# Kernel optimization log

Measured on AMD Instinct MI355X. Metric: run time of the kernel, lower is better.

## Reference

```python
import jax, jax.numpy as jnp
import numpy as np

H = 512          # hidden_size
B = 1024         # batch
T = 256          # warmup sequence length
NUM_STEPS = 64


def setup_inputs() -> dict:
    key = jax.random.key(0)
    ks = jax.random.split(key, 8)
    bound = 1.0 / np.sqrt(H)  # torch default init for RNN/Linear
    x = jax.random.normal(ks[0], (B, T), dtype=jnp.float32)
    W_ih = jax.random.uniform(ks[1], (H, 1), jnp.float32, -bound, bound)
    W_hh = jax.random.uniform(ks[2], (H, H), jnp.float32, -bound, bound)
    b_ih = jax.random.uniform(ks[3], (H,), jnp.float32, -bound, bound)
    b_hh = jax.random.uniform(ks[4], (H,), jnp.float32, -bound, bound)
    W_fc = jax.random.uniform(ks[5], (1, H), jnp.float32, -bound, bound)
    b_fc = jax.random.uniform(ks[6], (1,), jnp.float32, -bound, bound)
    return {"x": x, "W_ih": W_ih, "W_hh": W_hh, "b_ih": b_ih,
            "b_hh": b_hh, "W_fc": W_fc, "b_fc": b_fc, "num_steps": NUM_STEPS}


def reference(x, W_ih, W_hh, b_ih, b_hh, W_fc, b_fc, num_steps):
    # Phase 1: warmup RNN over the input series. h_t = relu(x_t*W_ih + b_ih + h@W_hh^T + b_hh)
    bias = b_ih + b_hh  # [H]
    w_in = W_ih[:, 0]   # [H], input_size == 1

    def warm_step(h, xt):                      # h: [B,H], xt: [B]
        h = jax.nn.relu(xt[:, None] * w_in[None, :] + h @ W_hh.T + bias)
        return h, None

    h0 = jnp.zeros((B, H), dtype=x.dtype)
    h, _ = jax.lax.scan(warm_step, h0, x.T)    # scan over time: x.T is [T,B]

    def roll_step(h, _):
        y = h @ W_fc.T + b_fc                  # [B,1]
        h = jax.nn.relu(y @ W_ih.T + h @ W_hh.T + bias)
        return h, y

    _, ys = jax.lax.scan(roll_step, h, None, length=num_steps)  # ys: [S,B,1]
    return jnp.transpose(ys, (1, 0, 2))        # [B, num_steps, 1]
```

## Files before the change

kernel.cpp:

```cpp
#include <hip/hip_runtime.h>
#include <stdint.h>

#define H 512
#define B_SZ 1024
#define T_WARM 256
#define NSTEPS 64
#define TOTAL_T (T_WARM + NSTEPS)

#define RPB 16
#define HC 128
#define NTEAM 64
#define NCG 4
#define NBLK 256
#define NTHR 512

typedef __attribute__((ext_vector_type(8))) short bf16x8;
typedef __attribute__((ext_vector_type(4))) float f32x4;

union u64x2_bf {
    uint64_t u[2];
    bf16x8 v;
};

__device__ __forceinline__ ushort f2bf(float f) {
    uint32_t u = __builtin_bit_cast(uint32_t, f);
    u += 0x7FFFu + ((u >> 16) & 1u);
    return (ushort)(u >> 16);
}
__device__ __forceinline__ float bf2f(ushort h) {
    uint32_t u = ((uint32_t)h) << 16;
    return __builtin_bit_cast(float, u);
}

__global__ void prep_kernel(const float* __restrict__ x,
                            const float* __restrict__ W_hh,
                            const float* __restrict__ b_ih,
                            const float* __restrict__ b_hh,
                            ushort* __restrict__ Wh, ushort* __restrict__ Wl,
                            float* __restrict__ bias, float* __restrict__ xT,
                            uint32_t* __restrict__ Hhi0, uint32_t* __restrict__ Hlo0,
                            uint32_t* __restrict__ flags) {
    int i = blockIdx.x * 512 + threadIdx.x;
    if (i < B_SZ * 256) { Hhi0[i] = 0u; Hlo0[i] = 0u; }
    if (i < 4096) flags[i] = 0u;
    if (i < H * H) {
        float w = W_hh[i];
        ushort hi = f2bf(w);
        float rem = w - bf2f(hi);
        Wh[i] = hi;
        Wl[i] = f2bf(rem);
    }
    if (i < B_SZ * T_WARM) {
        int b = i & (B_SZ - 1), t = i >> 10;
        xT[t * B_SZ + b] = x[b * T_WARM + t];
    }
    if (i < H) bias[i] = b_ih[i] + b_hh[i];
}

__global__ __launch_bounds__(NTHR, 1)
void rnn_kernel(const float* __restrict__ xT,
                const float* __restrict__ W_ih,
                const float* __restrict__ b_fc_p,
                const float* __restrict__ W_fc,
                const ushort* __restrict__ Wh_g,
                const ushort* __restrict__ Wl_g,
                const float* __restrict__ bias_g,
                uint32_t* __restrict__ Hhi0, uint32_t* __restrict__ Hhi1,
                uint32_t* __restrict__ Hlo0, uint32_t* __restrict__ Hlo1,
                uint32_t* __restrict__ flags,
                float* __restrict__ out) {
    __shared__ float pc[8 * 8 * 64 * 4];
    __shared__ float w_fc_s[H];
    __shared__ float w_in_s[HC];
    __shared__ float bias_s[HC];
    __shared__ float ypt[32 * 16];
    __shared__ float sx[RPB];
    __shared__ float sy[RPB];

    const int tid = threadIdx.x;
    const int bid = blockIdx.x;
    const int team = bid & (NTEAM - 1);
    const int cg = bid >> 6;
    const int row0 = team * RPB;
    const int col0 = cg * HC;

    w_fc_s[tid] = W_fc[tid];
    if (tid < HC) { w_in_s[tid] = W_ih[col0 + tid]; bias_s[tid] = bias_g[col0 + tid]; }
    const float bfc = b_fc_p[0];

    const int lane = tid & 63;
    const int wv = tid >> 6;
    const int n = lane & 15, q = lane >> 4;

    bf16x8 Bh[16], Bl[16];
    {
        const int kb = wv * 64 + q * 8;
        #pragma unroll
        for (int c = 0; c < 8; ++c) {
            const ushort* wh = Wh_g + (col0 + c * 16 + n) * H + kb;
            const ushort* wl = Wl_g + (col0 + c * 16 + n) * H + kb;
            Bh[c * 2 + 0] = *(const bf16x8*)(wh);
            Bh[c * 2 + 1] = *(const bf16x8*)(wh + 32);
            Bl[c * 2 + 0] = *(const bf16x8*)(wl);
            Bl[c * 2 + 1] = *(const bf16x8*)(wl + 32);
        }
    }

    uint32_t* myflag = flags + (team * NCG + cg) * 16;
    const uint32_t* pollflag = flags + (team * NCG + (wv >> 1)) * 16;
    const bool selfw = ((wv >> 1) == cg);

    for (int t = 0; t < TOTAL_T; ++t) {
        float xv = 0.f;
        if (t < T_WARM && tid < RPB) xv = xT[t * B_SZ + row0 + tid];

        if (t > 0 && !selfw) {
            while (__hip_atomic_load(pollflag, __ATOMIC_RELAXED, __HIP_MEMORY_SCOPE_AGENT)
                   < (uint32_t)t)
                __builtin_amdgcn_s_sleep(1);
        }

        const uint64_t* ph = (const uint64_t*)((t & 1) ? Hhi1 : Hhi0);
        const uint64_t* pl = (const uint64_t*)((t & 1) ? Hlo1 : Hlo0);
        const int abase = (row0 + n) * 128 + wv * 16 + q * 2;
        u64x2_bf ah[2], al[2];
        #pragma unroll
        for (int ktl = 0; ktl < 2; ++ktl) {
            ah[ktl].u[0] = __hip_atomic_load(ph + abase + ktl * 8 + 0, __ATOMIC_RELAXED, __HIP_MEMORY_SCOPE_AGENT);
            ah[ktl].u[1] = __hip_atomic_load(ph + abase + ktl * 8 + 1, __ATOMIC_RELAXED, __HIP_MEMORY_SCOPE_AGENT);
            al[ktl].u[0] = __hip_atomic_load(pl + abase + ktl * 8 + 0, __ATOMIC_RELAXED, __HIP_MEMORY_SCOPE_AGENT);
            al[ktl].u[1] = __hip_atomic_load(pl + abase + ktl * 8 + 1, __ATOMIC_RELAXED, __HIP_MEMORY_SCOPE_AGENT);
        }

        f32x4 acc[8];
        #pragma unroll
        for (int c = 0; c < 8; ++c) acc[c] = (f32x4){0.f, 0.f, 0.f, 0.f};
        #pragma unroll
        for (int ktl = 0; ktl < 2; ++ktl) {
            #pragma unroll
            for (int c = 0; c < 8; ++c) {
                acc[c] = __builtin_amdgcn_mfma_f32_16x16x32_bf16(ah[ktl].v, Bh[c * 2 + ktl], acc[c], 0, 0, 0);
                acc[c] = __builtin_amdgcn_mfma_f32_16x16x32_bf16(al[ktl].v, Bh[c * 2 + ktl], acc[c], 0, 0, 0);
                acc[c] = __builtin_amdgcn_mfma_f32_16x16x32_bf16(ah[ktl].v, Bl[c * 2 + ktl], acc[c], 0, 0, 0);
            }
        }

        #pragma unroll
        for (int c = 0; c < 8; ++c)
            *(f32x4*)(&pc[((wv * 8 + c) * 64 + lane) * 4]) = acc[c];
        if (t < T_WARM && tid < RPB) sx[tid] = xv;
        if (t >= T_WARM) {
            float yp = 0.f;
            #pragma unroll
            for (int ktl = 0; ktl < 2; ++ktl)
                #pragma unroll
                for (int j = 0; j < 8; ++j) {
                    int k = wv * 64 + ktl * 32 + q * 8 + j;
                    yp += (bf2f((ushort)ah[ktl].v[j]) + bf2f((ushort)al[ktl].v[j])) * w_fc_s[k];
                }
            ypt[(wv * 4 + q) * 16 + n] = yp;
        }
        __syncthreads();

        if (t >= T_WARM) {
            if (tid < RPB) {
                float s = bfc;
                #pragma unroll
                for (int g = 0; g < 32; ++g) s += ypt[g * 16 + tid];
                sy[tid] = s;
                if (cg == 0) out[(row0 + tid) * NSTEPS + (t - T_WARM)] = s;
            }
            __syncthreads();
        }

        f32x4 v = (f32x4){0.f, 0.f, 0.f, 0.f};
        #pragma unroll
        for (int w = 0; w < 8; ++w)
            v += *(const f32x4*)(&pc[((w * 8 + wv) * 64 + lane) * 4]);

        const int jl = wv * 16 + n;
        const float wi = w_in_s[jl], bj = bias_s[jl];
        uint32_t* dsth = ((t & 1) ? Hhi0 : Hhi1);
        uint32_t* dstl = ((t & 1) ? Hlo0 : Hlo1);
        const int pi = (col0 + jl) >> 1;
        #pragma unroll
        for (int i = 0; i < 4; ++i) {
            int m = q * 4 + i;
            float sv = (t < T_WARM) ? sx[m] : sy[m];
            float val = v[i] + sv * wi + bj;
            val = fmaxf(val, 0.f);
            ushort hi = f2bf(val);
            float rem = val - bf2f(hi);
            uint32_t mine = ((uint32_t)hi << 16) | (uint32_t)f2bf(rem);
            uint32_t partner = (uint32_t)__shfl_xor((int)mine, 1);
            int du = (row0 + m) * 256 + pi;
            if ((n & 1) == 0) {
                uint32_t hw = (mine >> 16) | (partner & 0xFFFF0000u);
                __hip_atomic_store(dsth + du, hw, __ATOMIC_RELAXED, __HIP_MEMORY_SCOPE_AGENT);
            } else {
                uint32_t lw = (partner & 0xFFFFu) | (mine << 16);
                __hip_atomic_store(dstl + du, lw, __ATOMIC_RELAXED, __HIP_MEMORY_SCOPE_AGENT);
            }
        }
        __syncthreads();
        if (tid == 0)
            __hip_atomic_store(myflag, (uint32_t)(t + 1), __ATOMIC_RELAXED, __HIP_MEMORY_SCOPE_AGENT);
    }
}

extern "C" void kernel_launch(void* const* d_in, const int* in_sizes, int n_in,
                              void* d_out, int out_size, void* d_ws, size_t ws_size,
                              hipStream_t stream) {
    const float* x    = (const float*)d_in[0];
    const float* W_ih = (const float*)d_in[1];
    const float* W_hh = (const float*)d_in[2];
    const float* b_ih = (const float*)d_in[3];
    const float* b_hh = (const float*)d_in[4];
    const float* W_fc = (const float*)d_in[5];
    const float* b_fc = (const float*)d_in[6];
    float* out = (float*)d_out;

    uint8_t* w = (uint8_t*)d_ws;
    ushort*   Wh    = (ushort*)(w);
    ushort*   Wl    = (ushort*)(w + 524288);
    float*    bias  = (float*)(w + 1048576);
    float*    xT    = (float*)(w + 1052672);
    uint32_t* Hhi0  = (uint32_t*)(w + 2101248);
    uint32_t* Hhi1  = (uint32_t*)(w + 3149824);
    uint32_t* Hlo0  = (uint32_t*)(w + 4198400);
    uint32_t* Hlo1  = (uint32_t*)(w + 5246976);
    uint32_t* flags = (uint32_t*)(w + 6295552);

    prep_kernel<<<1024, 512, 0, stream>>>(x, W_hh, b_ih, b_hh, Wh, Wl, bias, xT, Hhi0, Hlo0, flags);
    rnn_kernel<<<NBLK, NTHR, 0, stream>>>(xT, W_ih, b_fc, W_fc, Wh, Wl, bias,
                                          Hhi0, Hhi1, Hlo0, Hlo1, flags, out);
}
```

Measured before the change: 1.173 ms.

## Replace per-step flag barrier with tag-bit-validated hidden state polling

Drops the separate per-block progress flags and the trailing block barrier. Each hidden-state word now carries a parity tag in its top bit, and consumers spin on the data itself until every word shows the expected tag. The partial-sum LDS buffer is double-buffered to remove the end-of-step syncthreads, and x is broadcast by shuffle instead of through shared memory. This cuts a flag round-trip and a barrier from every step. In exchange the tag bit overwrites the sign bit of the hi/lo words, which relies on relu outputs being non-negative and on the residual's sign being recoverable, and state is stored unpacked and then repacked in registers.

```diff
diff --git a/kernel.cpp b/kernel.cpp
--- a/kernel.cpp
+++ b/kernel.cpp
@@ -17,10 +17,7 @@
 typedef __attribute__((ext_vector_type(8))) short bf16x8;
 typedef __attribute__((ext_vector_type(4))) float f32x4;
 
-union u64x2_bf {
-    uint64_t u[2];
-    bf16x8 v;
-};
+union u32x4_bf { uint32_t w[4]; bf16x8 v; };
 
 __device__ __forceinline__ ushort f2bf(float f) {
     uint32_t u = __builtin_bit_cast(uint32_t, f);
@@ -38,11 +35,10 @@
                             const float* __restrict__ b_hh,
                             ushort* __restrict__ Wh, ushort* __restrict__ Wl,
                             float* __restrict__ bias, float* __restrict__ xT,
-                            uint32_t* __restrict__ Hhi0, uint32_t* __restrict__ Hlo0,
-                            uint32_t* __restrict__ flags) {
+                            uint32_t* __restrict__ Hb0, uint32_t* __restrict__ Hb1) {
     int i = blockIdx.x * 512 + threadIdx.x;
-    if (i < B_SZ * 256) { Hhi0[i] = 0u; Hlo0[i] = 0u; }
-    if (i < 4096) flags[i] = 0u;
+    Hb0[i] = 0u;
+    Hb1[i] = 0x80000000u;
     if (i < H * H) {
         float w = W_hh[i];
         ushort hi = f2bf(w);
@@ -65,16 +61,13 @@
                 const ushort* __restrict__ Wh_g,
                 const ushort* __restrict__ Wl_g,
                 const float* __restrict__ bias_g,
-                uint32_t* __restrict__ Hhi0, uint32_t* __restrict__ Hhi1,
-                uint32_t* __restrict__ Hlo0, uint32_t* __restrict__ Hlo1,
-                uint32_t* __restrict__ flags,
+                uint32_t* __restrict__ Hb0, uint32_t* __restrict__ Hb1,
                 float* __restrict__ out) {
-    __shared__ float pc[8 * 8 * 64 * 4];
+    __shared__ float pc[2][8 * 8 * 64 * 4];
     __shared__ float w_fc_s[H];
     __shared__ float w_in_s[HC];
     __shared__ float bias_s[HC];
     __shared__ float ypt[32 * 16];
-    __shared__ float sx[RPB];
     __shared__ float sy[RPB];
 
     const int tid = threadIdx.x;
@@ -106,49 +99,59 @@
         }
     }
 
-    uint32_t* myflag = flags + (team * NCG + cg) * 16;
-    const uint32_t* pollflag = flags + (team * NCG + (wv >> 1)) * 16;
-    const bool selfw = ((wv >> 1) == cg);
+    const uint64_t TB = 0x8000000080000000ULL;
 
     for (int t = 0; t < TOTAL_T; ++t) {
         float xv = 0.f;
-        if (t < T_WARM && tid < RPB) xv = xT[t * B_SZ + row0 + tid];
-
-        if (t > 0 && !selfw) {
-            while (__hip_atomic_load(pollflag, __ATOMIC_RELAXED, __HIP_MEMORY_SCOPE_AGENT)
-                   < (uint32_t)t)
-                __builtin_amdgcn_s_sleep(1);
-        }
-
-        const uint64_t* ph = (const uint64_t*)((t & 1) ? Hhi1 : Hhi0);
-        const uint64_t* pl = (const uint64_t*)((t & 1) ? Hlo1 : Hlo0);
-        const int abase = (row0 + n) * 128 + wv * 16 + q * 2;
-        u64x2_bf ah[2], al[2];
-        #pragma unroll
-        for (int ktl = 0; ktl < 2; ++ktl) {
-            ah[ktl].u[0] = __hip_atomic_load(ph + abase + ktl * 8 + 0, __ATOMIC_RELAXED, __HIP_MEMORY_SCOPE_AGENT);
-            ah[ktl].u[1] = __hip_atomic_load(ph + abase + ktl * 8 + 1, __ATOMIC_RELAXED, __HIP_MEMORY_SCOPE_AGENT);
-            al[ktl].u[0] = __hip_atomic_load(pl + abase + ktl * 8 + 0, __ATOMIC_RELAXED, __HIP_MEMORY_SCOPE_AGENT);
-            al[ktl].u[1] = __hip_atomic_load(pl + abase + ktl * 8 + 1, __ATOMIC_RELAXED, __HIP_MEMORY_SCOPE_AGENT);
-        }
+        if (t < T_WARM && lane < RPB) xv = xT[t * B_SZ + row0 + lane];
+
+        const uint64_t* src = (const uint64_t*)((t & 1) ? Hb1 : Hb0);
+        const int base = (row0 + n) * 256 + wv * 32 + q * 4;
+        const uint64_t want = ((t >> 1) & 1) ? TB : 0ULL;
+        uint64_t d[8];
+        for (;;) {
+            #pragma unroll
+            for (int j = 0; j < 4; ++j)
+                d[j] = __hip_atomic_load(src + base + j, __ATOMIC_RELAXED, __HIP_MEMORY_SCOPE_AGENT);
+            #pragma unroll
+            for (int j = 0; j < 4; ++j)
+                d[4 + j] = __hip_atomic_load(src + base + 16 + j, __ATOMIC_RELAXED, __HIP_MEMORY_SCOPE_AGENT);
+            uint64_t bad = 0;
+            #pragma unroll
+            for (int j = 0; j < 8; ++j) bad |= (d[j] ^ want);
+            if (__all((bad & TB) == 0)) break;
+            __builtin_amdgcn_s_sleep(1);
+        }
+        #pragma unroll
+        for (int j = 0; j < 8; ++j) d[j] &= ~TB;
+
+        u32x4_bf ah[2], al[2];
+        #pragma unroll
+        for (int ktl = 0; ktl < 2; ++ktl)
+            #pragma unroll
+            for (int p = 0; p < 4; ++p) {
+                uint32_t lo32 = (uint32_t)d[ktl * 4 + p];
+                uint32_t hi32 = (uint32_t)(d[ktl * 4 + p] >> 32);
+                ah[ktl].w[p] = (lo32 >> 16) | (hi32 & 0xFFFF0000u);
+                al[ktl].w[p] = (lo32 & 0xFFFFu) | (hi32 << 16);
+            }
 
         f32x4 acc[8];
         #pragma unroll
         for (int c = 0; c < 8; ++c) acc[c] = (f32x4){0.f, 0.f, 0.f, 0.f};
         #pragma unroll
-        for (int ktl = 0; ktl < 2; ++ktl) {
+        for (int ktl = 0; ktl < 2; ++ktl)
             #pragma unroll
             for (int c = 0; c < 8; ++c) {
                 acc[c] = __builtin_amdgcn_mfma_f32_16x16x32_bf16(ah[ktl].v, Bh[c * 2 + ktl], acc[c], 0, 0, 0);
                 acc[c] = __builtin_amdgcn_mfma_f32_16x16x32_bf16(al[ktl].v, Bh[c * 2 + ktl], acc[c], 0, 0, 0);
                 acc[c] = __builtin_amdgcn_mfma_f32_16x16x32_bf16(ah[ktl].v, Bl[c * 2 + ktl], acc[c], 0, 0, 0);
             }
-        }
-
+
+        float* pcb = pc[t & 1];
         #pragma unroll
         for (int c = 0; c < 8; ++c)
-            *(f32x4*)(&pc[((wv * 8 + c) * 64 + lane) * 4]) = acc[c];
-        if (t < T_WARM && tid < RPB) sx[tid] = xv;
+            *(f32x4*)(&pcb[((wv * 8 + c) * 64 + lane) * 4]) = acc[c];
         if (t >= T_WARM) {
             float yp = 0.f;
             #pragma unroll
@@ -176,35 +179,24 @@
         f32x4 v = (f32x4){0.f, 0.f, 0.f, 0.f};
         #pragma unroll
         for (int w = 0; w < 8; ++w)
-            v += *(const f32x4*)(&pc[((w * 8 + wv) * 64 + lane) * 4]);
+            v += *(const f32x4*)(&pcb[((w * 8 + wv) * 64 + lane) * 4]);
 
         const int jl = wv * 16 + n;
         const float wi = w_in_s[jl], bj = bias_s[jl];
-        uint32_t* dsth = ((t & 1) ? Hhi0 : Hhi1);
-        uint32_t* dstl = ((t & 1) ? Hlo0 : Hlo1);
-        const int pi = (col0 + jl) >> 1;
+        uint32_t* dst = ((t & 1) ? Hb0 : Hb1);
+        const uint32_t tagw = (((t + 1) >> 1) & 1) ? 0x80000000u : 0u;
         #pragma unroll
         for (int i = 0; i < 4; ++i) {
             int m = q * 4 + i;
-            float sv = (t < T_WARM) ? sx[m] : sy[m];
+            float sv = (t < T_WARM) ? __shfl(xv, m) : sy[m];
             float val = v[i] + sv * wi + bj;
             val = fmaxf(val, 0.f);
             ushort hi = f2bf(val);
             float rem = val - bf2f(hi);
-            uint32_t mine = ((uint32_t)hi << 16) | (uint32_t)f2bf(rem);
-            uint32_t partner = (uint32_t)__shfl_xor((int)mine, 1);
-            int du = (row0 + m) * 256 + pi;
-            if ((n & 1) == 0) {
-                uint32_t hw = (mine >> 16) | (partner & 0xFFFF0000u);
-                __hip_atomic_store(dsth + du, hw, __ATOMIC_RELAXED, __HIP_MEMORY_SCOPE_AGENT);
-            } else {
-                uint32_t lw = (partner & 0xFFFFu) | (mine << 16);
-                __hip_atomic_store(dstl + du, lw, __ATOMIC_RELAXED, __HIP_MEMORY_SCOPE_AGENT);
-            }
-        }
-        __syncthreads();
-        if (tid == 0)
-            __hip_atomic_store(myflag, (uint32_t)(t + 1), __ATOMIC_RELAXED, __HIP_MEMORY_SCOPE_AGENT);
+            uint32_t u = (((uint32_t)hi << 16) | (uint32_t)f2bf(rem)) | tagw;
+            __hip_atomic_store(dst + (row0 + m) * H + col0 + jl, u,
+                               __ATOMIC_RELAXED, __HIP_MEMORY_SCOPE_AGENT);
+        }
     }
 }
 
@@ -221,17 +213,13 @@
     float* out = (float*)d_out;
 
     uint8_t* w = (uint8_t*)d_ws;
-    ushort*   Wh    = (ushort*)(w);
-    ushort*   Wl    = (ushort*)(w + 524288);
-    float*    bias  = (float*)(w + 1048576);
-    float*    xT    = (float*)(w + 1052672);
-    uint32_t* Hhi0  = (uint32_t*)(w + 2101248);
-    uint32_t* Hhi1  = (uint32_t*)(w + 3149824);
-    uint32_t* Hlo0  = (uint32_t*)(w + 4198400);
-    uint32_t* Hlo1  = (uint32_t*)(w + 5246976);
-    uint32_t* flags = (uint32_t*)(w + 6295552);
-
-    prep_kernel<<<1024, 512, 0, stream>>>(x, W_hh, b_ih, b_hh, Wh, Wl, bias, xT, Hhi0, Hlo0, flags);
-    rnn_kernel<<<NBLK, NTHR, 0, stream>>>(xT, W_ih, b_fc, W_fc, Wh, Wl, bias,
-                                          Hhi0, Hhi1, Hlo0, Hlo1, flags, out);
-}
+    ushort*   Wh   = (ushort*)(w);
+    ushort*   Wl   = (ushort*)(w + 524288);
+    float*    bias = (float*)(w + 1048576);
+    float*    xT   = (float*)(w + 1052672);
+    uint32_t* Hb0  = (uint32_t*)(w + 2101248);
+    uint32_t* Hb1  = (uint32_t*)(w + 4198400);
+
+    prep_kernel<<<1024, 512, 0, stream>>>(x, W_hh, b_ih, b_hh, Wh, Wl, bias, xT, Hb0, Hb1);
+    rnn_kernel<<<NBLK, NTHR, 0, stream>>>(xT, W_ih, b_fc, W_fc, Wh, Wl, bias, Hb0, Hb1, out);
+}
```

After: 1.950 ms. +66.2%, slower.
